# Optimization experiments

Hardware: AMD Instinct MI355X
Metric: run time of the kernel (lower is better)

## Reference

```python
import jax, jax.numpy as jnp
import numpy as np
import math

D = 1024; H = 16; HD = D // H; K = 8; NS = 512; G = D // 4
N_IN = D // 5; N_AT = int(D * 0.3); N_OUT = int(D * 0.3)
N_MO = D - N_IN - N_AT - N_OUT
M_IN = 4; M_AT = 128; M_OUT = 16; M_MO = 4; NLM_H = 16
B = 2; T = 512
T_IN = 2; T_MO = 2  # ticks_per_region: input/motor = max(2, K//8)


def _glu(z):
    a, b = jnp.split(z, 2, axis=-1)
    return a * jax.nn.sigmoid(b)


def _rms(x, eps=1e-6):
    return x * jax.lax.rsqrt(jnp.mean(x * x, axis=-1, keepdims=True) + eps)


def _ln(x, g, b, eps=1e-5):
    mu = jnp.mean(x, axis=-1, keepdims=True)
    var = jnp.mean((x - mu) ** 2, axis=-1, keepdims=True)
    return (x - mu) * jax.lax.rsqrt(var + eps) * g + b


def _nlm(tr, w, b):
    # tr: (BT, n, m); w: (m, o, n); b: (n, o) -> GLU-halved (BT, n, o/2)
    return _glu(jnp.einsum('bnm,mon->bno', tr, w) + b)


def _forward(x, Wq, Wk, Wv, Wg, W_in, ln_in_g, ln_in_b, W_at, ln_at_g, ln_at_b,
             W_out, ln_out_g, ln_out_b, W_mo, ln_mo_g, ln_mo_b, tick_embed,
             decay_out, decay_act, Wc, in_w1, in_b1, in_s0, in_tr0,
             at_w1, at_b1, at_w2, at_b2, at_s0, at_tr0,
             out_w1, out_b1, out_w2, out_b2, out_s0, out_tr0,
             mo_w1, mo_b1, mo_s0, mo_tr0,
             idx_out_l, idx_out_r, idx_act_l, idx_act_r):
    Bx, Tx, _ = x.shape
    BT = Bx * Tx
    kk = _rms((x @ Wk).reshape(Bx, Tx, H, HD))
    vv = (x @ Wv).reshape(Bx, Tx, H, HD)
    mask = jnp.tril(jnp.ones((Tx, Tx), dtype=bool))
    scale = 1.0 / math.sqrt(HD)

    state = jnp.broadcast_to(jnp.concatenate([in_s0, at_s0, out_s0, mo_s0]), (BT, D))
    tr_in = jnp.broadcast_to(in_tr0, (BT, N_IN, M_IN))
    tr_at = jnp.broadcast_to(at_tr0, (BT, N_AT, M_AT))
    tr_out = jnp.broadcast_to(out_tr0, (BT, N_OUT, M_OUT))
    tr_mo = jnp.broadcast_to(mo_tr0, (BT, N_MO, M_MO))

    alpha_out = state[:, idx_out_l] * state[:, idx_out_r]
    beta_out = jnp.ones_like(alpha_out)
    alpha_act = state[:, idx_act_l] * state[:, idx_act_r]
    beta_act = jnp.ones_like(alpha_act)
    d_out = jnp.exp(-jnp.clip(decay_out, 0.0, 15.0))
    d_act = jnp.exp(-jnp.clip(decay_act, 0.0, 15.0))

    s_in = state[:, :N_IN]
    s_at = state[:, N_IN:N_IN + N_AT]
    s_out = state[:, N_IN + N_AT:N_IN + N_AT + N_OUT]
    s_mo = state[:, N_IN + N_AT + N_OUT:]

    for t in range(K):  # fixed small tick count
        sync_act = alpha_act * jax.lax.rsqrt(beta_act)
        q = _rms((sync_act @ Wq).reshape(Bx, Tx, H, HD))
        sc = jnp.einsum('bqhd,bkhd->bhqk', q, kk) * scale
        sc = jnp.where(mask, sc, -1e30)
        attn = jnp.einsum('bhqk,bkhd->bqhd', jax.nn.softmax(sc, axis=-1), vv)
        attn = attn.reshape(BT, D) + tick_embed[t]
        gfeat = _glu(state @ Wg)

        if t < T_IN:
            pre = _ln(_glu(jnp.concatenate([attn, s_mo, gfeat], -1) @ W_in), ln_in_g, ln_in_b)
            tr_in = jnp.concatenate([tr_in[:, :, 1:], pre[:, :, None]], -1)
            s_in = _nlm(tr_in, in_w1, in_b1)[..., 0]

        pre = _ln(_glu(jnp.concatenate([s_in, attn], -1) @ W_at), ln_at_g, ln_at_b)
        tr_at = jnp.concatenate([tr_at[:, :, 1:], pre[:, :, None]], -1)
        s_at = _nlm(_nlm(tr_at, at_w1, at_b1), at_w2, at_b2)[..., 0]

        pre = _ln(_glu(jnp.concatenate([s_at, attn, gfeat], -1) @ W_out), ln_out_g, ln_out_b)
        tr_out = jnp.concatenate([tr_out[:, :, 1:], pre[:, :, None]], -1)
        s_out = _nlm(_nlm(tr_out, out_w1, out_b1), out_w2, out_b2)[..., 0]

        if t < T_MO:
            pre = _ln(_glu(jnp.concatenate([s_out, gfeat], -1) @ W_mo), ln_mo_g, ln_mo_b)
            tr_mo = jnp.concatenate([tr_mo[:, :, 1:], pre[:, :, None]], -1)
            s_mo = _nlm(tr_mo, mo_w1, mo_b1)[..., 0]

        state = jnp.concatenate([s_in, s_at, s_out, s_mo], -1)
        alpha_out = d_out * alpha_out + state[:, idx_out_l] * state[:, idx_out_r]
        beta_out = d_out * beta_out + 1.0
        alpha_act = d_act * alpha_act + state[:, idx_act_l] * state[:, idx_act_r]
        beta_act = d_act * beta_act + 1.0

    sync_out = alpha_out * jax.lax.rsqrt(beta_out)
    return (sync_out @ Wc).reshape(Bx, Tx, D)


def setup_inputs():
    key = jax.random.key(0)
    ki = iter(jax.random.split(key, 64))
    s = (3.0 ** 0.5) * (D ** -0.5) * 0.68

    def un(shape, sc):
        return jax.random.uniform(next(ki), shape, jnp.float32, -sc, sc)

    def sl(m, o, n):  # SuperLinear: w (m,o,n), b zeros (n,o)
        sc = 1.0 / math.sqrt(m + o)
        return un((m, o, n), sc), jnp.zeros((n, o), jnp.float32)

    inp = {}
    inp['x'] = jax.random.normal(next(ki), (B, T, D), jnp.float32)
    inp['Wq'] = un((NS, D), s); inp['Wk'] = un((D, D), s); inp['Wv'] = un((D, D), s)
    inp['Wg'] = un((D, 2 * G), s)
    inp['W_in'] = un((D + N_MO + G, 2 * N_IN), s)
    inp['ln_in_g'] = jnp.ones(N_IN); inp['ln_in_b'] = jnp.zeros(N_IN)
    inp['W_at'] = un((N_IN + D, 2 * N_AT), s)
    inp['ln_at_g'] = jnp.ones(N_AT); inp['ln_at_b'] = jnp.zeros(N_AT)
    inp['W_out'] = un((N_AT + D + G, 2 * N_OUT), s)
    inp['ln_out_g'] = jnp.ones(N_OUT); inp['ln_out_b'] = jnp.zeros(N_OUT)
    inp['W_mo'] = un((N_OUT + G, 2 * N_MO), s)
    inp['ln_mo_g'] = jnp.ones(N_MO); inp['ln_mo_b'] = jnp.zeros(N_MO)
    inp['tick_embed'] = jax.random.normal(next(ki), (K, D), jnp.float32) * 0.02
    inp['decay_out'] = jnp.zeros(NS, jnp.float32)
    inp['decay_act'] = jnp.zeros(NS, jnp.float32)
    inp['Wc'] = un((NS, D), s)
    inp['in_w1'], inp['in_b1'] = sl(M_IN, 2, N_IN)
    inp['in_s0'] = un((N_IN,), math.sqrt(1.0 / N_IN))
    inp['in_tr0'] = un((N_IN, M_IN), math.sqrt(1.0 / (N_IN + M_IN)))
    inp['at_w1'], inp['at_b1'] = sl(M_AT, 2 * NLM_H, N_AT)
    inp['at_w2'], inp['at_b2'] = sl(NLM_H, 2, N_AT)
    inp['at_s0'] = un((N_AT,), math.sqrt(1.0 / N_AT))
    inp['at_tr0'] = un((N_AT, M_AT), math.sqrt(1.0 / (N_AT + M_AT)))
    inp['out_w1'], inp['out_b1'] = sl(M_OUT, 2 * NLM_H, N_OUT)
    inp['out_w2'], inp['out_b2'] = sl(NLM_H, 2, N_OUT)
    inp['out_s0'] = un((N_OUT,), math.sqrt(1.0 / N_OUT))
    inp['out_tr0'] = un((N_OUT, M_OUT), math.sqrt(1.0 / (N_OUT + M_OUT)))
    inp['mo_w1'], inp['mo_b1'] = sl(M_MO, 2, N_MO)
    inp['mo_s0'] = un((N_MO,), math.sqrt(1.0 / N_MO))
    inp['mo_tr0'] = un((N_MO, M_MO), math.sqrt(1.0 / (N_MO + M_MO)))
    inp['idx_out_l'] = jax.random.permutation(next(ki), D)[:NS].astype(jnp.int32)
    inp['idx_out_r'] = jax.random.permutation(next(ki), D)[:NS].astype(jnp.int32)
    inp['idx_act_l'] = jax.random.permutation(next(ki), D)[:NS].astype(jnp.int32)
    inp['idx_act_r'] = jax.random.permutation(next(ki), D)[:NS].astype(jnp.int32)
    return inp


def reference(x, Wq, Wk, Wv, Wg, W_in, ln_in_g, ln_in_b, W_at, ln_at_g, ln_at_b,
              W_out, ln_out_g, ln_out_b, W_mo, ln_mo_g, ln_mo_b, tick_embed,
              decay_out, decay_act, Wc, in_w1, in_b1, in_s0, in_tr0,
              at_w1, at_b1, at_w2, at_b2, at_s0, at_tr0,
              out_w1, out_b1, out_w2, out_b2, out_s0, out_tr0,
              mo_w1, mo_b1, mo_s0, mo_tr0,
              idx_out_l, idx_out_r, idx_act_l, idx_act_r):
    return _forward(x, Wq, Wk, Wv, Wg, W_in, ln_in_g, ln_in_b, W_at, ln_at_g, ln_at_b,
                    W_out, ln_out_g, ln_out_b, W_mo, ln_mo_g, ln_mo_b, tick_embed,
                    decay_out, decay_act, Wc, in_w1, in_b1, in_s0, in_tr0,
                    at_w1, at_b1, at_w2, at_b2, at_s0, at_tr0,
                    out_w1, out_b1, out_w2, out_b2, out_s0, out_tr0,
                    mo_w1, mo_b1, mo_s0, mo_tr0,
                    idx_out_l, idx_out_r, idx_act_l, idx_act_r)
```

## Files before the change

kernel.cpp:

```cpp
#include <hip/hip_runtime.h>
#include <hip/hip_bf16.h>
#include <math.h>

typedef __hip_bfloat16 bf16;
typedef short v8s __attribute__((ext_vector_type(8)));
typedef float v4f __attribute__((ext_vector_type(4)));

__device__ __forceinline__ float B2F(bf16 x) { return __bfloat162float(x); }
__device__ __forceinline__ float sigm(float x) { return 1.0f / (1.0f + expf(-x)); }

__device__ __forceinline__ void split2(float v, short& hi, short& lo) {
    unsigned u = __float_as_uint(v);
    hi = (short)(u >> 16);
    float r = v - __uint_as_float(u & 0xFFFF0000u);
    bf16 l = __float2bfloat16(r);
    short ls; __builtin_memcpy(&ls, &l, 2);
    lo = ls;
}

__device__ __forceinline__ float loadAny(const void* src, size_t off, bool bf) {
    return bf ? B2F(((const bf16*)src)[off]) : ((const float*)src)[off];
}

static constexpr int D_    = 1024;
static constexpr int H_    = 16;
static constexpr int KT_   = 8;
static constexpr int NS_   = 512;
static constexpr int G_    = 256;
static constexpr int NIN_  = 204;
static constexpr int NAT_  = 307;
static constexpr int NOUT_ = 307;
static constexpr int NMO_  = 206;
static constexpr int B_    = 2;
static constexpr int T_    = 512;
static constexpr int BT_   = 1024;
static constexpr int NF_   = 41;
static constexpr int NW_   = 9;
static constexpr int NC_   = 31;

static constexpr int LAT_ = 1248;
static constexpr int LOU_ = 1600;
static constexpr int LIN_ = 1504;
static constexpr int LMO_ = 576;

struct CvtArgs { const void* src[NC_]; long long dstOff[NC_]; long long cum[NC_ + 1]; };

__global__ void detect_kernel(const void* probe, int* flag) {
    if (threadIdx.x == 0 && blockIdx.x == 0) {
        unsigned u = *(const unsigned*)probe;
        *flag = (u == 0x3F803F80u) ? 1 : 0;
    }
}

__global__ void cvt_all_kernel(CvtArgs a, float* __restrict__ dst,
                               const int* __restrict__ flag, long long total) {
    long long i0 = ((long long)blockIdx.x * 256 + threadIdx.x) * 4;
    if (i0 >= total) return;
    int lo = 0, hi = NC_;
    while (hi - lo > 1) { int mid = (lo + hi) >> 1; if (a.cum[mid] <= i0) lo = mid; else hi = mid; }
    bool bf = (*flag != 0);
    #pragma unroll
    for (int k = 0; k < 4; ++k) {
        long long i = i0 + k;
        if (i >= total) break;
        if (i >= a.cum[lo + 1]) ++lo;
        long long off = i - a.cum[lo];
        dst[a.dstOff[lo] + off] = loadAny(a.src[lo], off, bf);
    }
}

__global__ void final_any_kernel(const float* __restrict__ src, void* dst,
                                 const int* __restrict__ flag, int n) {
    int i = blockIdx.x * blockDim.x + threadIdx.x;
    if (i >= n) return;
    if (*flag) ((bf16*)dst)[i] = __float2bfloat16(src[i]);
    else       ((float*)dst)[i] = src[i];
}

__global__ void split_x_kernel(const void* __restrict__ src, const int* __restrict__ flag,
                               short* __restrict__ dh, short* __restrict__ dl, int n) {
    int i = blockIdx.x * blockDim.x + threadIdx.x;
    if (i >= n) return;
    float v = loadAny(src, i, *flag != 0);
    short h, l; split2(v, h, l);
    dh[i] = h; dl[i] = l;
}

__global__ void zeropad_kernel(short* zath, short* zatl, short* zouth, short* zoutl,
                               short* zinh, short* zinl, short* zmoh, short* zmol) {
    int r = blockIdx.x, j = threadIdx.x;
    if (j < 20)      { zath[(size_t)r * LAT_ + 1228 + j] = 0; zatl[(size_t)r * LAT_ + 1228 + j] = 0; }
    else if (j < 33) { zouth[(size_t)r * LOU_ + 1587 + (j - 20)] = 0; zoutl[(size_t)r * LOU_ + 1587 + (j - 20)] = 0; }
    else if (j < 51) { zinh[(size_t)r * LIN_ + 1486 + (j - 33)] = 0; zinl[(size_t)r * LIN_ + 1486 + (j - 33)] = 0; }
    else             { zmoh[(size_t)r * LMO_ + 563 + (j - 51)] = 0; zmol[(size_t)r * LMO_ + 563 + (j - 51)] = 0; }
}

struct TD { const void* src; long long dstOff; int K, N, ldk; };
struct TDs { TD d[NW_]; };

__global__ __launch_bounds__(256)
void transpose_split_kernel(const int* __restrict__ flag,
                            short* __restrict__ wth, short* __restrict__ wtl, TDs tds)
{
    TD d = tds.d[blockIdx.z];
    if (d.N == 0) return;
    int k0 = blockIdx.y * 32, n0 = blockIdx.x * 32;
    if (k0 >= d.ldk || n0 >= d.N) return;
    __shared__ float T[32][33];
    bool bf = (*flag != 0);
    int r = threadIdx.x >> 5, cc = threadIdx.x & 31;
    #pragma unroll
    for (int rr = 0; rr < 4; ++rr) {
        int k = k0 + r + rr * 8;
        int n = n0 + cc;
        float v = 0.f;
        if (k < d.K && n < d.N) v = loadAny(d.src, (size_t)k * d.N + n, bf);
        T[r + rr * 8][cc] = v;
    }
    __syncthreads();
    #pragma unroll
    for (int rr = 0; rr < 4; ++rr) {
        int n = n0 + r + rr * 8;
        int k = k0 + cc;
        if (n < d.N) {
            short hi, lo;
            split2(T[cc][r + rr * 8], hi, lo);
            wth[d.dstOff + (size_t)n * d.ldk + k] = hi;
            wtl[d.dstOff + (size_t)n * d.ldk + k] = lo;
        }
    }
}

__global__ __launch_bounds__(256)
void wg_pack_kernel(const void* __restrict__ src, const int* __restrict__ flag,
                    short* __restrict__ wth, short* __restrict__ wtl)
{
    int n0 = blockIdx.x * 32;
    int k0 = blockIdx.y * 32;
    __shared__ float T[32][33];
    bool bf = (*flag != 0);
    int r = threadIdx.x >> 5, cc = threadIdx.x & 31;
    int dng = n0 + cc;
    int nsrc = (dng & 1) ? (G_ + (dng >> 1)) : (dng >> 1);
    #pragma unroll
    for (int rr = 0; rr < 4; ++rr) {
        int k = k0 + r + rr * 8;
        T[r + rr * 8][cc] = loadAny(src, (size_t)k * 512 + nsrc, bf);
    }
    __syncthreads();
    #pragma unroll
    for (int rr = 0; rr < 4; ++rr) {
        int dn = n0 + r + rr * 8;
        int k = k0 + cc;
        short hi, lo;
        split2(T[cc][r + rr * 8], hi, lo);
        wth[(size_t)dn * 1024 + k] = hi;
        wtl[(size_t)dn * 1024 + k] = lo;
    }
}

__global__ void nlm_repack_kernel(const float* __restrict__ w1, const float* __restrict__ w2,
                                  int n, int Mdim,
                                  float* __restrict__ w1d, float* __restrict__ w2t) {
    int idx = blockIdx.x * blockDim.x + threadIdx.x;
    int tot1 = 8 * n * 32;
    if (idx < tot1) {
        int o = idx & 31;
        int rest = idx >> 5;
        int i = rest % n;
        int dt = rest / n;
        w1d[((size_t)dt * n + i) * 32 + o] = w1[((size_t)(Mdim - 8 + dt) * 32 + o) * n + i];
    } else if (idx < tot1 + n * 32) {
        int j = idx - tot1;
        int o = j & 31;
        int i = j >> 5;
        w2t[(size_t)i * 32 + o] = w2[(size_t)o * n + i];
    }
}

__global__ __launch_bounds__(256)
void gemm_mfma_kernel(const short* __restrict__ Ah, const short* __restrict__ Al, int lda_s,
                      const short* __restrict__ WTh, const short* __restrict__ WTl, int ldk,
                      float* __restrict__ C, int ldc, size_t pstride, int N,
                      int KC, int nCh, const int* __restrict__ flag)
{
    __shared__ short AhS[2048], AlS[2048], WhS[2048], WlS[2048];
    const int tid = threadIdx.x;
    const int lane = tid & 63;
    const int wave = tid >> 6;
    const int wm = (wave >> 1) * 32, wn = (wave & 1) * 32;
    const int m0 = blockIdx.y * 64, n0 = blockIdx.x * 64;
    const bool wlo = (*flag == 0);
    v4f acc[2][2] = {};

    const int srow = (tid >> 6) * 16 + (tid & 15);
    const int skoff = ((tid >> 4) & 3) * 8;
    const short* ArowH = Ah + (size_t)(m0 + srow) * lda_s + skoff;
    const short* ArowL = Al + (size_t)(m0 + srow) * lda_s + skoff;
    const int wrow = n0 + srow;
    const bool wv = wrow < N;
    const short* WrowH = WTh + (size_t)(wv ? wrow : 0) * ldk + skoff;
    const short* WrowL = WTl + (size_t)(wv ? wrow : 0) * ldk + skoff;

    const int aoff = ((wm >> 4) * 64 + lane) * 8;
    const int boff = ((wn >> 4) * 64 + lane) * 8;
    const int fr = lane & 15;

    const int c0 = blockIdx.z * KC;
    const int c1 = min(nCh, c0 + KC);

    v8s pAh, pAl, pWh, pWl = {};
    {
        const int k0 = c0 << 5;
        pAh = *(const v8s*)(ArowH + k0);
        pAl = *(const v8s*)(ArowL + k0);
        pWh = (v8s){};
        if (wv) pWh = *(const v8s*)(WrowH + k0);
        if (wlo && wv) pWl = *(const v8s*)(WrowL + k0);
    }

    for (int c = c0; c < c1; ++c) {
        __syncthreads();
        *(v8s*)&AhS[tid * 8] = pAh;
        *(v8s*)&AlS[tid * 8] = pAl;
        *(v8s*)&WhS[tid * 8] = pWh;
        if (wlo) *(v8s*)&WlS[tid * 8] = pWl;
        if (c + 1 < c1) {
            const int k0 = (c + 1) << 5;
            pAh = *(const v8s*)(ArowH + k0);
            pAl = *(const v8s*)(ArowL + k0);
            pWh = (v8s){};
            if (wv) pWh = *(const v8s*)(WrowH + k0);
            if (wlo && wv) pWl = *(const v8s*)(WrowL + k0);
        }
        __syncthreads();
        v8s a_h[2], a_l[2], b_h[2];
        a_h[0] = *(v8s*)&AhS[aoff];
        a_h[1] = *(v8s*)&AhS[aoff + 512];
        a_l[0] = *(v8s*)&AlS[aoff];
        a_l[1] = *(v8s*)&AlS[aoff + 512];
        b_h[0] = *(v8s*)&WhS[boff];
        b_h[1] = *(v8s*)&WhS[boff + 512];
        #pragma unroll
        for (int i = 0; i < 2; ++i)
            #pragma unroll
            for (int j = 0; j < 2; ++j) {
                acc[i][j] = __builtin_amdgcn_mfma_f32_16x16x32_bf16(a_h[i], b_h[j], acc[i][j], 0, 0, 0);
                acc[i][j] = __builtin_amdgcn_mfma_f32_16x16x32_bf16(a_l[i], b_h[j], acc[i][j], 0, 0, 0);
            }
        if (wlo) {
            v8s b_l[2];
            b_l[0] = *(v8s*)&WlS[boff];
            b_l[1] = *(v8s*)&WlS[boff + 512];
            #pragma unroll
            for (int i = 0; i < 2; ++i)
                #pragma unroll
                for (int j = 0; j < 2; ++j)
                    acc[i][j] = __builtin_amdgcn_mfma_f32_16x16x32_bf16(a_h[i], b_l[j], acc[i][j], 0, 0, 0);
        }
    }
    float* Cs = C + (size_t)blockIdx.z * pstride;
    #pragma unroll
    for (int j = 0; j < 2; ++j) {
        int col = n0 + wn + j * 16 + fr;
        if (col < N) {
            #pragma unroll
            for (int i = 0; i < 2; ++i)
                #pragma unroll
                for (int r = 0; r < 4; ++r) {
                    int row = m0 + wm + i * 16 + (lane >> 4) * 4 + r;
                    Cs[(size_t)row * ldc + col] = acc[i][j][r];
                }
        }
    }
}

__global__ __launch_bounds__(256)
void rms_kpack_kernel(const float* __restrict__ kvb,
                      short* __restrict__ kh, short* __restrict__ kl) {
    int r = blockIdx.x * 4 + (threadIdx.x >> 6);
    int d = threadIdx.x & 63;
    int h = r & 15, key = (r >> 4) & 511, b = r >> 13;
    float v = kvb[(size_t)(b * 512 + key) * 2048 + h * 64 + d];
    float ss = v * v;
    #pragma unroll
    for (int o = 32; o > 0; o >>= 1) ss += __shfl_xor(ss, o);
    v *= 1.0f / sqrtf(ss * (1.0f / 64.0f) + 1e-6f);
    short hh, ll; split2(v, hh, ll);
    int bh = b * 16 + h;
    int kc = key >> 6, t4 = (key & 63) >> 4, f = key & 15;
    int ks = d >> 5, q = (d >> 3) & 3, j = d & 7;
    size_t o_ = (size_t)bh * 32768 + kc * 4096 + (((t4 * 2 + ks) * 64 + q * 16 + f) * 8) + j;
    kh[o_] = hh; kl[o_] = ll;
}

__global__ void vpack_kernel(const float* __restrict__ kvb,
                             short* __restrict__ vh, short* __restrict__ vl) {
    int idx = blockIdx.x * blockDim.x + threadIdx.x;
    if (idx >= 32 * 512 * 64) return;
    int d = idx & 63;
    int key = (idx >> 6) & 511;
    int bh = idx >> 15;
    int b = bh >> 4, h = bh & 15;
    float v = kvb[(size_t)(b * 512 + key) * 2048 + 1024 + h * 64 + d];
    short hh, ll; split2(v, hh, ll);
    int kc = key >> 6;
    int kk2 = key & 63;
    int ks = kk2 >> 5, q = (kk2 >> 3) & 3, j = kk2 & 7;
    int t4 = d >> 4, f = d & 15;
    size_t o = (size_t)bh * 32768 + kc * 4096 + (((t4 * 2 + ks) * 64 + q * 16 + f) * 8) + j;
    vh[o] = hh; vl[o] = ll;
}

__global__ void init_state_kernel(const float* __restrict__ s_in0, const float* __restrict__ s_at0,
                                  const float* __restrict__ s_out0, const float* __restrict__ s_mo0,
                                  float* __restrict__ state,
                                  short* __restrict__ sth, short* __restrict__ stl,
                                  short* __restrict__ zath, short* __restrict__ zatl,
                                  short* __restrict__ zouth, short* __restrict__ zoutl,
                                  short* __restrict__ zinh, short* __restrict__ zinl,
                                  short* __restrict__ zmoh, short* __restrict__ zmol) {
    int idx = blockIdx.x * blockDim.x + threadIdx.x;
    if (idx >= BT_ * D_) return;
    int b = idx >> 10;
    int i = idx & (D_ - 1);
    float v;
    if (i < NIN_) v = s_in0[i];
    else if (i < NIN_ + NAT_) v = s_at0[i - NIN_];
    else if (i < NIN_ + NAT_ + NOUT_) v = s_out0[i - NIN_ - NAT_];
    else v = s_mo0[i - NIN_ - NAT_ - NOUT_];
    state[idx] = v;
    short h, l; split2(v, h, l);
    sth[idx] = h; stl[idx] = l;
    if (i < NIN_) { zath[(size_t)b * LAT_ + i] = h; zatl[(size_t)b * LAT_ + i] = l; }
    else if (i < NIN_ + NAT_) {
        zouth[(size_t)b * LOU_ + (i - NIN_)] = h; zoutl[(size_t)b * LOU_ + (i - NIN_)] = l;
    } else if (i < NIN_ + NAT_ + NOUT_) {
        zmoh[(size_t)b * LMO_ + (i - NIN_ - NAT_)] = h; zmol[(size_t)b * LMO_ + (i - NIN_ - NAT_)] = l;
    } else {
        zinh[(size_t)b * LIN_ + 1024 + (i - NIN_ - NAT_ - NOUT_)] = h;
        zinl[(size_t)b * LIN_ + 1024 + (i - NIN_ - NAT_ - NOUT_)] = l;
    }
}

__global__ void decay_kernel(const float* __restrict__ d_o, const float* __restrict__ d_a,
                             float* __restrict__ eo, float* __restrict__ ea) {
    int j = blockIdx.x * blockDim.x + threadIdx.x;
    if (j >= NS_) return;
    float x = d_o[j]; x = fminf(fmaxf(x, 0.f), 15.f); eo[j] = expf(-x);
    float y = d_a[j]; y = fminf(fmaxf(y, 0.f), 15.f); ea[j] = expf(-y);
}

__global__ void init_sync_kernel(const float* __restrict__ state,
                                 const int* __restrict__ ol, const int* __restrict__ orr,
                                 const int* __restrict__ al, const int* __restrict__ ar,
                                 float* __restrict__ ao, float* __restrict__ bo,
                                 float* __restrict__ aa, float* __restrict__ ba,
                                 short* __restrict__ sbh, short* __restrict__ sbl) {
    int idx = blockIdx.x * blockDim.x + threadIdx.x;
    if (idx >= BT_ * NS_) return;
    int b = idx >> 9;
    int j = idx & (NS_ - 1);
    const float* st = state + (size_t)b * D_;
    float vo = st[ol[j]] * st[orr[j]];
    float va = st[al[j]] * st[ar[j]];
    ao[idx] = vo; bo[idx] = 1.f;
    aa[idx] = va; ba[idx] = 1.f;
    short h, l; split2(va, h, l);
    sbh[idx] = h; sbl[idx] = l;
}

__global__ void syncupd_kernel(const float* __restrict__ state,
                               const float* __restrict__ eo, const float* __restrict__ ea,
                               const int* __restrict__ ol, const int* __restrict__ orr,
                               const int* __restrict__ al, const int* __restrict__ ar,
                               float* __restrict__ ao, float* __restrict__ bo,
                               float* __restrict__ aa, float* __restrict__ ba,
                               short* __restrict__ sbh, short* __restrict__ sbl) {
    int idx = blockIdx.x * blockDim.x + threadIdx.x;
    if (idx >= BT_ * NS_) return;
    int b = idx >> 9;
    int j = idx & (NS_ - 1);
    const float* st = state + (size_t)b * D_;
    float d = eo[j];
    ao[idx] = d * ao[idx] + st[ol[j]] * st[orr[j]];
    bo[idx] = d * bo[idx] + 1.f;
    d = ea[j];
    float a2 = d * aa[idx] + st[al[j]] * st[ar[j]];
    float b2 = d * ba[idx] + 1.f;
    aa[idx] = a2; ba[idx] = b2;
    float v = a2 / sqrtf(b2);
    short h, l; split2(v, h, l);
    sbh[idx] = h; sbl[idx] = l;
}

__global__ void syncact_split_kernel(const float* __restrict__ a, const float* __restrict__ be,
                                     short* __restrict__ oh, short* __restrict__ olo) {
    int idx = blockIdx.x * blockDim.x + threadIdx.x;
    if (idx >= BT_ * NS_) return;
    float v = a[idx] / sqrtf(be[idx]);
    short h, l; split2(v, h, l);
    oh[idx] = h; olo[idx] = l;
}

__global__ __launch_bounds__(256)
void attn_mfma_kernel(const float* __restrict__ qpart, int qsplits, size_t qps,
                      const short* __restrict__ kh_g, const short* __restrict__ kl_g,
                      const short* __restrict__ vh_g, const short* __restrict__ vl_g,
                      const float* __restrict__ te,
                      short* __restrict__ zath, short* __restrict__ zatl,
                      short* __restrict__ zouth, short* __restrict__ zoutl,
                      short* __restrict__ zinh, short* __restrict__ zinl, int wr_in)
{
    __shared__ short kksh[4096], kksl[4096];
    __shared__ short vtsh[4096], vtsl[4096];
    __shared__ short psh[4][1024], psl[4][1024];

    const int bid = blockIdx.x;
    const int bh = bid >> 3, qbk = bid & 7;
    const int b = bh >> 4, h = bh & 15;
    const int q0 = qbk * 64;
    const int tid = threadIdx.x, w = tid >> 6, lane = tid & 63;
    const int quad = lane >> 4, fr = lane & 15;

    const int qrow = q0 + w * 16 + fr;
    const size_t qoffg = ((size_t)(b * T_ + qrow)) * D_ + h * 64 + quad * 8;
    float qv[16];
    #pragma unroll
    for (int j = 0; j < 8; ++j) { qv[j] = qpart[qoffg + j]; qv[8 + j] = qpart[qoffg + 32 + j]; }
    for (int s = 1; s < qsplits; ++s) {
        const float* qp = qpart + (size_t)s * qps + qoffg;
        #pragma unroll
        for (int j = 0; j < 8; ++j) { qv[j] += qp[j]; qv[8 + j] += qp[32 + j]; }
    }
    float ss = 0.f;
    #pragma unroll
    for (int j = 0; j < 16; ++j) ss += qv[j] * qv[j];
    ss += __shfl_xor(ss, 16);
    ss += __shfl_xor(ss, 32);
    const float qsc = (1.0f / sqrtf(ss * (1.0f / 64.0f) + 1e-6f)) * 0.125f;
    v8s qh[2], ql[2];
    #pragma unroll
    for (int ks = 0; ks < 2; ++ks)
        #pragma unroll
        for (int j = 0; j < 8; ++j) {
            short hh, ll; split2(qv[ks * 8 + j] * qsc, hh, ll);
            qh[ks][j] = hh; ql[ks][j] = ll;
        }

    v4f oacc[4] = {};
    float m_[4], l_[4];
    #pragma unroll
    for (int r = 0; r < 4; ++r) { m_[r] = -INFINITY; l_[r] = 0.f; }

    const size_t kvbase = (size_t)bh * 32768;
    const int s0 = tid * 8, s1 = (tid + 256) * 8;

    v8s pk0, pk1, pkl0, pkl1, pv0, pv1, pvl0, pvl1;
    {
        const size_t cb = kvbase;
        pk0  = *(const v8s*)&kh_g[cb + s0]; pk1  = *(const v8s*)&kh_g[cb + s1];
        pkl0 = *(const v8s*)&kl_g[cb + s0]; pkl1 = *(const v8s*)&kl_g[cb + s1];
        pv0  = *(const v8s*)&vh_g[cb + s0]; pv1  = *(const v8s*)&vh_g[cb + s1];
        pvl0 = *(const v8s*)&vl_g[cb + s0]; pvl1 = *(const v8s*)&vl_g[cb + s1];
    }

    for (int c = 0; c <= qbk; ++c) {
        __syncthreads();
        *(v8s*)&kksh[s0] = pk0;  *(v8s*)&kksh[s1] = pk1;
        *(v8s*)&kksl[s0] = pkl0; *(v8s*)&kksl[s1] = pkl1;
        *(v8s*)&vtsh[s0] = pv0;  *(v8s*)&vtsh[s1] = pv1;
        *(v8s*)&vtsl[s0] = pvl0; *(v8s*)&vtsl[s1] = pvl1;
        if (c < qbk) {
            const size_t cb = kvbase + (size_t)(c + 1) * 4096;
            pk0  = *(const v8s*)&kh_g[cb + s0]; pk1  = *(const v8s*)&kh_g[cb + s1];
            pkl0 = *(const v8s*)&kl_g[cb + s0]; pkl1 = *(const v8s*)&kl_g[cb + s1];
            pv0  = *(const v8s*)&vh_g[cb + s0]; pv1  = *(const v8s*)&vh_g[cb + s1];
            pvl0 = *(const v8s*)&vl_g[cb + s0]; pvl1 = *(const v8s*)&vl_g[cb + s1];
        }
        __syncthreads();

        v4f sv[4] = {};
        #pragma unroll
        for (int ks = 0; ks < 2; ++ks) {
            #pragma unroll
            for (int t4 = 0; t4 < 4; ++t4) {
                int so = ((t4 * 2 + ks) * 64 + lane) * 8;
                v8s bh_ = *(v8s*)&kksh[so];
                v8s bl_ = *(v8s*)&kksl[so];
                sv[t4] = __builtin_amdgcn_mfma_f32_16x16x32_bf16(qh[ks], bh_, sv[t4], 0, 0, 0);
                sv[t4] = __builtin_amdgcn_mfma_f32_16x16x32_bf16(ql[ks], bh_, sv[t4], 0, 0, 0);
                sv[t4] = __builtin_amdgcn_mfma_f32_16x16x32_bf16(qh[ks], bl_, sv[t4], 0, 0, 0);
            }
        }

        const int kb = c * 64;
        #pragma unroll
        for (int r = 0; r < 4; ++r) {
            int qg = q0 + w * 16 + quad * 4 + r;
            float rm = -INFINITY;
            #pragma unroll
            for (int t4 = 0; t4 < 4; ++t4) {
                int key = kb + t4 * 16 + fr;
                float s = sv[t4][r];
                if (key > qg) s = -1e30f;
                sv[t4][r] = s;
                rm = fmaxf(rm, s);
            }
            rm = fmaxf(rm, __shfl_xor(rm, 1));
            rm = fmaxf(rm, __shfl_xor(rm, 2));
            rm = fmaxf(rm, __shfl_xor(rm, 4));
            rm = fmaxf(rm, __shfl_xor(rm, 8));
            float mn = fmaxf(m_[r], rm);
            float rs = 0.f;
            #pragma unroll
            for (int t4 = 0; t4 < 4; ++t4) {
                float p = __expf(sv[t4][r] - mn);
                sv[t4][r] = p;
                rs += p;
            }
            rs += __shfl_xor(rs, 1);
            rs += __shfl_xor(rs, 2);
            rs += __shfl_xor(rs, 4);
            rs += __shfl_xor(rs, 8);
            float al = __expf(m_[r] - mn);
            l_[r] = l_[r] * al + rs;
            m_[r] = mn;
            #pragma unroll
            for (int t4 = 0; t4 < 4; ++t4) oacc[t4][r] *= al;
            #pragma unroll
            for (int t4 = 0; t4 < 4; ++t4) {
                short hh, ll; split2(sv[t4][r], hh, ll);
                int po = (((t4 >> 1) * 4 + ((t4 & 1) * 2 + (fr >> 3))) * 16 + quad * 4 + r) * 8 + (fr & 7);
                psh[w][po] = hh;
                psl[w][po] = ll;
            }
        }

        #pragma unroll
        for (int ks = 0; ks < 2; ++ks) {
            int pa = (ks * 64 + lane) * 8;
            v8s ah_ = *(v8s*)&psh[w][pa];
            v8s al_ = *(v8s*)&psl[w][pa];
            #pragma unroll
            for (int t4 = 0; t4 < 4; ++t4) {
                int so = ((t4 * 2 + ks) * 64 + lane) * 8;
                v8s bh_ = *(v8s*)&vtsh[so];
                v8s bl_ = *(v8s*)&vtsl[so];
                oacc[t4] = __builtin_amdgcn_mfma_f32_16x16x32_bf16(ah_, bh_, oacc[t4], 0, 0, 0);
                oacc[t4] = __builtin_amdgcn_mfma_f32_16x16x32_bf16(al_, bh_, oacc[t4], 0, 0, 0);
                oacc[t4] = __builtin_amdgcn_mfma_f32_16x16x32_bf16(ah_, bl_, oacc[t4], 0, 0, 0);
            }
        }
    }

    #pragma unroll
    for (int t4 = 0; t4 < 4; ++t4) {
        float tev = te[h * 64 + t4 * 16 + fr];
        int col = h * 64 + t4 * 16 + fr;
        #pragma unroll
        for (int r = 0; r < 4; ++r) {
            int row = q0 + w * 16 + quad * 4 + r;
            size_t rb = (size_t)(b * T_ + row);
            float val = oacc[t4][r] / l_[r] + tev;
            short hh, ll; split2(val, hh, ll);
            zath[rb * LAT_ + NIN_ + col] = hh; zatl[rb * LAT_ + NIN_ + col] = ll;
            zouth[rb * LOU_ + NAT_ + col] = hh; zoutl[rb * LOU_ + NAT_ + col] = ll;
            if (wr_in) { zinh[rb * LIN_ + col] = hh; zinl[rb * LIN_ + col] = ll; }
        }
    }
}

__global__ void glu_sum_kernel(const float* __restrict__ p, int S, size_t pstride,
                               short* __restrict__ zouth, short* __restrict__ zoutl,
                               short* __restrict__ zinh, short* __restrict__ zinl,
                               short* __restrict__ zmoh, short* __restrict__ zmol, int wr2) {
    int idx = blockIdx.x * blockDim.x + threadIdx.x;
    if (idx >= BT_ * G_) return;
    int row = idx >> 8, j = idx & 255;
    float a = 0.f, bb = 0.f;
    for (int s = 0; s < S; ++s) {
        const float* pr = p + (size_t)s * pstride + (size_t)row * 512;
        a += pr[2 * j];
        bb += pr[2 * j + 1];
    }
    float gf = a * sigm(bb);
    short hh, ll; split2(gf, hh, ll);
    zouth[(size_t)row * LOU_ + 1331 + j] = hh; zoutl[(size_t)row * LOU_ + 1331 + j] = ll;
    if (wr2) {
        zinh[(size_t)row * LIN_ + 1230 + j] = hh; zinl[(size_t)row * LIN_ + 1230 + j] = ll;
        zmoh[(size_t)row * LMO_ + NOUT_ + j] = hh; zmol[(size_t)row * LMO_ + NOUT_ + j] = ll;
    }
}

__global__ __launch_bounds__(256)
void glu_ln_nlm_big_kernel(const float* __restrict__ z, size_t pstride, int n,
                           const float* __restrict__ g, const float* __restrict__ bb,
                           float* __restrict__ preBase, int t,
                           const float* __restrict__ st, const float* __restrict__ w1d,
                           const float* __restrict__ b1, const float* __restrict__ w2t,
                           const float* __restrict__ b2,
                           float* __restrict__ state, short* __restrict__ sth,
                           short* __restrict__ stl, int soff,
                           short* __restrict__ czh, short* __restrict__ czl,
                           int ldz, int catoff)
{
    __shared__ float preLDS[320];
    __shared__ float red[256];
    const int row = blockIdx.x;
    const float* zr = z + (size_t)row * 2 * n;
    float v[2];
    float lsum = 0.f;
    {
        int s = 0;
        for (int i = threadIdx.x; i < n; i += 256, ++s) {
            float a = zr[i] + zr[pstride + i] + zr[2 * pstride + i] + zr[3 * pstride + i];
            float gt = zr[n + i] + zr[pstride + n + i] + zr[2 * pstride + n + i] + zr[3 * pstride + n + i];
            float val = a * sigm(gt);
            v[s] = val;
            lsum += val;
        }
    }
    red[threadIdx.x] = lsum;
    __syncthreads();
    for (int sd = 128; sd > 0; sd >>= 1) {
        if (threadIdx.x < sd) red[threadIdx.x] += red[threadIdx.x + sd];
        __syncthreads();
    }
    float mu = red[0] / n;
    __syncthreads();
    float lss = 0.f;
    {
        int s = 0;
        for (int i = threadIdx.x; i < n; i += 256, ++s) { float dv = v[s] - mu; lss += dv * dv; }
    }
    red[threadIdx.x] = lss;
    __syncthreads();
    for (int sd = 128; sd > 0; sd >>= 1) {
        if (threadIdx.x < sd) red[threadIdx.x] += red[threadIdx.x + sd];
        __syncthreads();
    }
    float inv = 1.f / sqrtf(red[0] / n + 1e-5f);
    {
        int s = 0;
        for (int i = threadIdx.x; i < n; i += 256, ++s) {
            float pre = (v[s] - mu) * inv * g[i] + bb[i];
            preLDS[i] = pre;
            preBase[((size_t)t * BT_ + row) * n + i] = pre;
        }
    }
    __syncthreads();
    const int i_loc = threadIdx.x >> 3;
    const int og = threadIdx.x & 7;
    const int npass = (n + 31) >> 5;
    for (int p = 0; p < npass; ++p) {
        const int i = p * 32 + i_loc;
        if (i < n) {
            float4 h4;
            {
                float4 a = *((const float4*)(st + ((size_t)t * n + i) * 32) + og);
                float4 bq = *((const float4*)(b1 + (size_t)i * 32) + og);
                h4.x = a.x + bq.x; h4.y = a.y + bq.y; h4.z = a.z + bq.z; h4.w = a.w + bq.w;
            }
            for (int s = 0; s <= t; ++s) {
                float pv = (s < t) ? preBase[((size_t)s * BT_ + row) * n + i] : preLDS[i];
                float4 wq = *((const float4*)(w1d + ((size_t)(7 - t + s) * n + i) * 32) + og);
                h4.x += pv * wq.x; h4.y += pv * wq.y; h4.z += pv * wq.z; h4.w += pv * wq.w;
            }
            float4 hp;
            hp.x = __shfl_xor(h4.x, 4); hp.y = __shfl_xor(h4.y, 4);
            hp.z = __shfl_xor(h4.z, 4); hp.w = __shfl_xor(h4.w, 4);
            float h20 = 0.f, h21 = 0.f;
            if (og < 4) {
                float gv0 = h4.x * sigm(hp.x);
                float gv1 = h4.y * sigm(hp.y);
                float gv2 = h4.z * sigm(hp.z);
                float gv3 = h4.w * sigm(hp.w);
                const float4* w2v = (const float4*)(w2t + (size_t)i * 32) + og * 2;
                float4 w2a = w2v[0], w2b = w2v[1];
                h20 = gv0 * w2a.x + gv1 * w2a.z + gv2 * w2b.x + gv3 * w2b.z;
                h21 = gv0 * w2a.y + gv1 * w2a.w + gv2 * w2b.y + gv3 * w2b.w;
            }
            h20 += __shfl_xor(h20, 1); h21 += __shfl_xor(h21, 1);
            h20 += __shfl_xor(h20, 2); h21 += __shfl_xor(h21, 2);
            if (og == 0) {
                h20 += b2[i * 2]; h21 += b2[i * 2 + 1];
                float res = h20 * sigm(h21);
                size_t so = (size_t)row * D_ + soff + i;
                state[so] = res;
                short hh, ll; split2(res, hh, ll);
                sth[so] = hh; stl[so] = ll;
                czh[(size_t)row * ldz + catoff + i] = hh;
                czl[(size_t)row * ldz + catoff + i] = ll;
            }
        }
    }
}

__global__ __launch_bounds__(256)
void glu_ln_nlm_small_kernel(const float* __restrict__ z, size_t pstride, int n,
                             const float* __restrict__ g, const float* __restrict__ bb,
                             float* __restrict__ preBase, int t,
                             const float* __restrict__ tr0, const float* __restrict__ w1,
                             const float* __restrict__ b1,
                             float* __restrict__ state, short* __restrict__ sth,
                             short* __restrict__ stl, int soff,
                             short* __restrict__ czh, short* __restrict__ czl,
                             int ldz, int catoff)
{
    __shared__ float preLDS[320];
    __shared__ float red[256];
    const int row = blockIdx.x;
    const float* zr = z + (size_t)row * 2 * n;
    float v[2];
    float lsum = 0.f;
    {
        int s = 0;
        for (int i = threadIdx.x; i < n; i += 256, ++s) {
            float a = zr[i] + zr[pstride + i] + zr[2 * pstride + i] + zr[3 * pstride + i];
            float gt = zr[n + i] + zr[pstride + n + i] + zr[2 * pstride + n + i] + zr[3 * pstride + n + i];
            float val = a * sigm(gt);
            v[s] = val;
            lsum += val;
        }
    }
    red[threadIdx.x] = lsum;
    __syncthreads();
    for (int sd = 128; sd > 0; sd >>= 1) {
        if (threadIdx.x < sd) red[threadIdx.x] += red[threadIdx.x + sd];
        __syncthreads();
    }
    float mu = red[0] / n;
    __syncthreads();
    float lss = 0.f;
    {
        int s = 0;
        for (int i = threadIdx.x; i < n; i += 256, ++s) { float dv = v[s] - mu; lss += dv * dv; }
    }
    red[threadIdx.x] = lss;
    __syncthreads();
    for (int sd = 128; sd > 0; sd >>= 1) {
        if (threadIdx.x < sd) red[threadIdx.x] += red[threadIdx.x + sd];
        __syncthreads();
    }
    float inv = 1.f / sqrtf(red[0] / n + 1e-5f);
    {
        int s = 0;
        for (int i = threadIdx.x; i < n; i += 256, ++s) {
            float pre = (v[s] - mu) * inv * g[i] + bb[i];
            preLDS[i] = pre;
            preBase[((size_t)t * BT_ + row) * n + i] = pre;
        }
    }
    __syncthreads();
    for (int i = threadIdx.x; i < n; i += 256) {
        float win[4];
        if (t == 0) {
            win[0] = tr0[i * 4 + 1]; win[1] = tr0[i * 4 + 2]; win[2] = tr0[i * 4 + 3];
            win[3] = preLDS[i];
        } else {
            win[0] = tr0[i * 4 + 2]; win[1] = tr0[i * 4 + 3];
            win[2] = preBase[(size_t)row * n + i];
            win[3] = preLDS[i];
        }
        float h0 = b1[i * 2], h1 = b1[i * 2 + 1];
        #pragma unroll
        for (int mm = 0; mm < 4; ++mm) {
            h0 += win[mm] * w1[(size_t)(mm * 2 + 0) * n + i];
            h1 += win[mm] * w1[(size_t)(mm * 2 + 1) * n + i];
        }
        float res = h0 * sigm(h1);
        size_t so = (size_t)row * D_ + soff + i;
        state[so] = res;
        short hh, ll; split2(res, hh, ll);
        sth[so] = hh; stl[so] = ll;
        czh[(size_t)row * ldz + catoff + i] = hh;
        czl[(size_t)row * ldz + catoff + i] = ll;
    }
}

__global__ __launch_bounds__(256)
void static_nlm_kernel(const float* __restrict__ tr0, const float* __restrict__ w1,
                       float* __restrict__ st, int n, int Mdim)
{
    __shared__ float ws[127 * 32];
    __shared__ float trs[128];
    const int i = blockIdx.x;
    const int tid = threadIdx.x;
    const int nw = (Mdim - 1) * 32;
    for (int idx = tid; idx < nw; idx += 256)
        ws[idx] = w1[(size_t)idx * n + i];
    if (tid < Mdim) trs[tid] = tr0[(size_t)i * Mdim + tid];
    __syncthreads();
    const int t = tid >> 5, o = tid & 31;
    float h = 0.f;
    for (int j = 0; j + t + 1 < Mdim; ++j)
        h += trs[j + t + 1] * ws[j * 32 + o];
    st[((size_t)t * n + i) * 32 + o] = h;
}

extern "C" void kernel_launch(void* const* d_in, const int* in_sizes, int n_in,
                              void* d_out, int out_size, void* d_ws, size_t ws_size,
                              hipStream_t stream)
{
    const int* idx_ol = (const int*)d_in[41];
    const int* idx_or = (const int*)d_in[42];
    const int* idx_al = (const int*)d_in[43];
    const int* idx_ar = (const int*)d_in[44];

    size_t off = 0;
    auto alloc = [&](size_t ne) {
        float* r = (float*)d_ws + off;
        off += (ne + 63) & ~(size_t)63;
        return r;
    };
    int* flag = (int*)alloc(64);

    long long fcum[NF_ + 1];
    fcum[0] = 0;
    for (int i = 0; i < NF_; ++i) fcum[i + 1] = fcum[i] + in_sizes[i];
    float* stage = alloc((size_t)fcum[NF_]);
    auto SP = [&](int i) { return (const float*)(stage + fcum[i]); };

    const int cIdx[NC_] = {6, 7, 9, 10, 12, 13, 15, 16, 17, 18, 19,
                           21, 22, 23, 24, 25, 26, 27, 28, 29, 30,
                           31, 32, 33, 34, 35, 36, 37, 38, 39, 40};
    CvtArgs ca;
    long long ccum = 0;
    for (int i = 0; i < NC_; ++i) {
        int gi = cIdx[i];
        ca.src[i] = d_in[gi];
        ca.dstOff[i] = fcum[gi];
        ca.cum[i] = ccum;
        ccum += in_sizes[gi];
    }
    ca.cum[NC_] = ccum;

    const int wIdx[NW_] = {1, 2, 3, 4, 5, 8, 11, 14, 20};
    const int wK[NW_]   = {512, 1024, 1024, 1024, 1486, 1228, 1587, 563, 512};
    const int wN[NW_]   = {1024, 1024, 1024, 512, 408, 614, 614, 412, 1024};
    const int wS[NW_]   = {2, 1, 1, 4, 4, 4, 4, 4, 1};
    int ldkA[NW_];
    long long wOff[NW_];
    long long totS = 0;
    for (int i = 0; i < NW_; ++i) {
        ldkA[i] = (wK[i] + 31) & ~31;
        wOff[i] = totS;
        totS += (long long)wN[i] * ldkA[i];
    }
    short* wtH = (short*)alloc((size_t)(totS + 1) / 2 + 64);
    short* wtL = (short*)alloc((size_t)(totS + 1) / 2 + 64);

    short* xh     = (short*)alloc((size_t)BT_ * D_ / 2 + 64);
    short* xl     = (short*)alloc((size_t)BT_ * D_ / 2 + 64);
    short* sbh    = (short*)alloc((size_t)BT_ * NS_ / 2 + 64);
    short* sbl    = (short*)alloc((size_t)BT_ * NS_ / 2 + 64);
    short* sobh   = (short*)alloc((size_t)BT_ * NS_ / 2 + 64);
    short* sobl   = (short*)alloc((size_t)BT_ * NS_ / 2 + 64);
    short* sth    = (short*)alloc((size_t)BT_ * D_ / 2 + 64);
    short* stl    = (short*)alloc((size_t)BT_ * D_ / 2 + 64);
    short* khp    = (short*)alloc((size_t)32 * 512 * 64 / 2 + 64);
    short* klp    = (short*)alloc((size_t)32 * 512 * 64 / 2 + 64);
    short* vhp    = (short*)alloc((size_t)32 * 512 * 64 / 2 + 64);
    short* vlp    = (short*)alloc((size_t)32 * 512 * 64 / 2 + 64);
    short* zath   = (short*)alloc((size_t)BT_ * LAT_ / 2 + 64);
    short* zatl   = (short*)alloc((size_t)BT_ * LAT_ / 2 + 64);
    short* zouth  = (short*)alloc((size_t)BT_ * LOU_ / 2 + 64);
    short* zoutl  = (short*)alloc((size_t)BT_ * LOU_ / 2 + 64);
    short* zinh   = (short*)alloc((size_t)BT_ * LIN_ / 2 + 64);
    short* zinl   = (short*)alloc((size_t)BT_ * LIN_ / 2 + 64);
    short* zmoh   = (short*)alloc((size_t)BT_ * LMO_ / 2 + 64);
    short* zmol   = (short*)alloc((size_t)BT_ * LMO_ / 2 + 64);

    float* pbuf   = alloc((size_t)4 * BT_ * 1024);
    float* kvb    = alloc((size_t)BT_ * 2048);
    float* state  = alloc((size_t)BT_ * D_);
    float* ao     = alloc((size_t)BT_ * NS_);
    float* bo     = alloc((size_t)BT_ * NS_);
    float* aa     = alloc((size_t)BT_ * NS_);
    float* ba     = alloc((size_t)BT_ * NS_);
    float* eo     = alloc(NS_);
    float* ea     = alloc(NS_);
    float* pre_at = alloc((size_t)KT_ * BT_ * NAT_);
    float* pre_out= alloc((size_t)KT_ * BT_ * NOUT_);
    float* pre_in = alloc((size_t)2 * BT_ * NIN_);
    float* pre_mo = alloc((size_t)2 * BT_ * NMO_);
    float* st_at  = alloc((size_t)KT_ * NAT_ * 32);
    float* st_out = alloc((size_t)KT_ * NOUT_ * 32);
    float* w1d_at = alloc((size_t)8 * NAT_ * 32);
    float* w1d_out= alloc((size_t)8 * NOUT_ * 32);
    float* w2t_at = alloc((size_t)NAT_ * 32);
    float* w2t_out= alloc((size_t)NOUT_ * 32);
    float* outf   = alloc((size_t)BT_ * D_);
    (void)ws_size; (void)n_in; (void)out_size;

    detect_kernel<<<1, 64, 0, stream>>>(d_in[6], flag);
    cvt_all_kernel<<<(int)((ccum / 4 + 255) / 256) + 1, 256, 0, stream>>>(ca, stage, flag, ccum);
    zeropad_kernel<<<BT_, 64, 0, stream>>>(zath, zatl, zouth, zoutl, zinh, zinl, zmoh, zmol);
    {
        TDs tds;
        for (int i = 0; i < NW_; ++i) {
            int N = (i == 3) ? 0 : wN[i];
            tds.d[i] = TD{d_in[wIdx[i]], wOff[i], wK[i], N, ldkA[i]};
        }
        dim3 g(32, 50, NW_);
        transpose_split_kernel<<<g, 256, 0, stream>>>(flag, wtH, wtL, tds);
    }
    wg_pack_kernel<<<dim3(16, 32), 256, 0, stream>>>(d_in[4], flag, wtH + wOff[3], wtL + wOff[3]);

    const float* ln_in_g  = SP(6);
    const float* ln_in_b  = SP(7);
    const float* ln_at_g  = SP(9);
    const float* ln_at_b  = SP(10);
    const float* ln_out_g = SP(12);
    const float* ln_out_b = SP(13);
    const float* ln_mo_g  = SP(15);
    const float* ln_mo_b  = SP(16);
    const float* te       = SP(17);
    const float* dec_o    = SP(18);
    const float* dec_a    = SP(19);
    const float* in_w1    = SP(21);
    const float* in_b1    = SP(22);
    const float* in_s0    = SP(23);
    const float* in_tr0   = SP(24);
    const float* at_w1    = SP(25);
    const float* at_b1    = SP(26);
    const float* at_w2    = SP(27);
    const float* at_b2    = SP(28);
    const float* at_s0    = SP(29);
    const float* at_tr0   = SP(30);
    const float* out_w1   = SP(31);
    const float* out_b1   = SP(32);
    const float* out_w2   = SP(33);
    const float* out_b2   = SP(34);
    const float* out_s0   = SP(35);
    const float* out_tr0  = SP(36);
    const float* mo_w1    = SP(37);
    const float* mo_b1    = SP(38);
    const float* mo_s0    = SP(39);
    const float* mo_tr0   = SP(40);

    auto gemm = [&](const short* Ah, const short* Al, int lda_s, int wi,
                    float* C, int ldc) {
        int nCh = ldkA[wi] >> 5;
        int S = wS[wi];
        int KC = (nCh + S - 1) / S;
        dim3 g((wN[wi] + 63) / 64, BT_ / 64, S);
        gemm_mfma_kernel<<<g, 256, 0, stream>>>(Ah, Al, lda_s, wtH + wOff[wi], wtL + wOff[wi],
                                                ldkA[wi], C, ldc, (size_t)BT_ * ldc,
                                                wN[wi], KC, nCh, flag);
    };

    split_x_kernel<<<(BT_ * D_) / 256, 256, 0, stream>>>(d_in[0], flag, xh, xl, BT_ * D_);
    {
        dim3 g(2048 / 64, BT_ / 64, 1);
        gemm_mfma_kernel<<<g, 256, 0, stream>>>(xh, xl, 1024, wtH + wOff[1], wtL + wOff[1],
                                                1024, kvb, 2048, 0, 2048, 32, 32, flag);
    }
    rms_kpack_kernel<<<(B_ * T_ * H_) / 4, 256, 0, stream>>>(kvb, khp, klp);
    vpack_kernel<<<(32 * 512 * 64) / 256, 256, 0, stream>>>(kvb, vhp, vlp);
    init_state_kernel<<<(BT_ * D_) / 256, 256, 0, stream>>>(in_s0, at_s0, out_s0, mo_s0,
                                                            state, sth, stl,
                                                            zath, zatl, zouth, zoutl,
                                                            zinh, zinl, zmoh, zmol);
    decay_kernel<<<2, 256, 0, stream>>>(dec_o, dec_a, eo, ea);
    init_sync_kernel<<<(BT_ * NS_) / 256, 256, 0, stream>>>(state, idx_ol, idx_or, idx_al, idx_ar,
                                                            ao, bo, aa, ba, sbh, sbl);
    static_nlm_kernel<<<NAT_, 256, 0, stream>>>(at_tr0, at_w1, st_at, NAT_, 128);
    static_nlm_kernel<<<NOUT_, 256, 0, stream>>>(out_tr0, out_w1, st_out, NOUT_, 16);
    nlm_repack_kernel<<<(9 * NAT_ * 32 + 255) / 256, 256, 0, stream>>>(at_w1, at_w2, NAT_, 128,
                                                                       w1d_at, w2t_at);
    nlm_repack_kernel<<<(9 * NOUT_ * 32 + 255) / 256, 256, 0, stream>>>(out_w1, out_w2, NOUT_, 16,
                                                                        w1d_out, w2t_out);

    for (int t = 0; t < KT_; ++t) {
        gemm(sbh, sbl, 512, 0, pbuf, 1024);
        attn_mfma_kernel<<<256, 256, 0, stream>>>(pbuf, 2, (size_t)BT_ * 1024,
                                                  khp, klp, vhp, vlp, te + (size_t)t * D_,
                                                  zath, zatl, zouth, zoutl, zinh, zinl, (t < 2));
        gemm(sth, stl, 1024, 3, pbuf, 512);
        glu_sum_kernel<<<(BT_ * G_) / 256, 256, 0, stream>>>(pbuf, 4, (size_t)BT_ * 512,
                                                             zouth, zoutl, zinh, zinl,
                                                             zmoh, zmol, (t < 2));
        if (t < 2) {
            gemm(zinh, zinl, LIN_, 4, pbuf, 2 * NIN_);
            glu_ln_nlm_small_kernel<<<BT_, 256, 0, stream>>>(
                pbuf, (size_t)BT_ * 2 * NIN_, NIN_, ln_in_g, ln_in_b, pre_in, t,
                in_tr0, in_w1, in_b1, state, sth, stl, 0, zath, zatl, LAT_, 0);
        }
        gemm(zath, zatl, LAT_, 5, pbuf, 2 * NAT_);
        glu_ln_nlm_big_kernel<<<BT_, 256, 0, stream>>>(
            pbuf, (size_t)BT_ * 2 * NAT_, NAT_, ln_at_g, ln_at_b, pre_at, t,
            st_at, w1d_at, at_b1, w2t_at, at_b2, state, sth, stl, NIN_,
            zouth, zoutl, LOU_, 0);
        gemm(zouth, zoutl, LOU_, 6, pbuf, 2 * NOUT_);
        glu_ln_nlm_big_kernel<<<BT_, 256, 0, stream>>>(
            pbuf, (size_t)BT_ * 2 * NOUT_, NOUT_, ln_out_g, ln_out_b, pre_out, t,
            st_out, w1d_out, out_b1, w2t_out, out_b2, state, sth, stl, NIN_ + NAT_,
            zmoh, zmol, LMO_, 0);
        if (t < 2) {
            gemm(zmoh, zmol, LMO_, 7, pbuf, 2 * NMO_);
            glu_ln_nlm_small_kernel<<<BT_, 256, 0, stream>>>(
                pbuf, (size_t)BT_ * 2 * NMO_, NMO_, ln_mo_g, ln_mo_b, pre_mo, t,
                mo_tr0, mo_w1, mo_b1, state, sth, stl, NIN_ + NAT_ + NOUT_,
                zinh, zinl, LIN_, 1024);
        }
        syncupd_kernel<<<(BT_ * NS_) / 256, 256, 0, stream>>>(state, eo, ea, idx_ol, idx_or,
                                                              idx_al, idx_ar, ao, bo, aa, ba, sbh, sbl);
    }

    syncact_split_kernel<<<(BT_ * NS_) / 256, 256, 0, stream>>>(ao, bo, sobh, sobl);
    gemm(sobh, sobl, 512, 8, outf, 1024);
    final_any_kernel<<<(BT_ * D_) / 256, 256, 0, stream>>>(outf, d_out, flag, BT_ * D_);
}
```

Measured before the change: 1.646 ms.

## Process two rows per block in GLU-LN-NLM big kernel to reuse weights

Each block now handles two token rows. Two wavefronts do the GLU+LayerNorm with wave-level shuffle reductions instead of LDS tree reductions. In the NLM phase the per-neuron weight loads (w1d history taps, st, b1, w2) are hoisted and shared across both rows, which halves weight traffic and cuts block-level barriers. The cost is half as many blocks, so there is less parallelism to hide latency, and more registers are used for the cached float4 weights.

```diff
diff --git a/kernel.cpp b/kernel.cpp
--- a/kernel.cpp
+++ b/kernel.cpp
@@ -605,93 +605,92 @@
                            short* __restrict__ czh, short* __restrict__ czl,
                            int ldz, int catoff)
 {
-    __shared__ float preLDS[320];
-    __shared__ float red[256];
-    const int row = blockIdx.x;
-    const float* zr = z + (size_t)row * 2 * n;
-    float v[2];
-    float lsum = 0.f;
-    {
-        int s = 0;
-        for (int i = threadIdx.x; i < n; i += 256, ++s) {
+    __shared__ float preLDS[2][320];
+    const int tid = threadIdx.x;
+    const int wvid = tid >> 6, lane = tid & 63;
+    const int row0 = blockIdx.x * 2;
+
+    if (wvid < 2) {
+        const int row = row0 + wvid;
+        const float* zr = z + (size_t)row * 2 * n;
+        float v[6];
+        float lsum = 0.f;
+        int cnt = 0;
+        for (int i = lane; i < n; i += 64, ++cnt) {
             float a = zr[i] + zr[pstride + i] + zr[2 * pstride + i] + zr[3 * pstride + i];
             float gt = zr[n + i] + zr[pstride + n + i] + zr[2 * pstride + n + i] + zr[3 * pstride + n + i];
             float val = a * sigm(gt);
-            v[s] = val;
+            v[cnt] = val;
             lsum += val;
         }
-    }
-    red[threadIdx.x] = lsum;
+        #pragma unroll
+        for (int o = 32; o > 0; o >>= 1) lsum += __shfl_xor(lsum, o);
+        float mu = lsum / n;
+        float lss = 0.f;
+        for (int c = 0; c < cnt; ++c) { float dv = v[c] - mu; lss += dv * dv; }
+        #pragma unroll
+        for (int o = 32; o > 0; o >>= 1) lss += __shfl_xor(lss, o);
+        float inv = 1.f / sqrtf(lss / n + 1e-5f);
+        int c = 0;
+        for (int i = lane; i < n; i += 64, ++c) {
+            float pre = (v[c] - mu) * inv * g[i] + bb[i];
+            preLDS[wvid][i] = pre;
+            preBase[((size_t)t * BT_ + row) * n + i] = pre;
+        }
+    }
     __syncthreads();
-    for (int sd = 128; sd > 0; sd >>= 1) {
-        if (threadIdx.x < sd) red[threadIdx.x] += red[threadIdx.x + sd];
-        __syncthreads();
-    }
-    float mu = red[0] / n;
-    __syncthreads();
-    float lss = 0.f;
-    {
-        int s = 0;
-        for (int i = threadIdx.x; i < n; i += 256, ++s) { float dv = v[s] - mu; lss += dv * dv; }
-    }
-    red[threadIdx.x] = lss;
-    __syncthreads();
-    for (int sd = 128; sd > 0; sd >>= 1) {
-        if (threadIdx.x < sd) red[threadIdx.x] += red[threadIdx.x + sd];
-        __syncthreads();
-    }
-    float inv = 1.f / sqrtf(red[0] / n + 1e-5f);
-    {
-        int s = 0;
-        for (int i = threadIdx.x; i < n; i += 256, ++s) {
-            float pre = (v[s] - mu) * inv * g[i] + bb[i];
-            preLDS[i] = pre;
-            preBase[((size_t)t * BT_ + row) * n + i] = pre;
-        }
-    }
-    __syncthreads();
-    const int i_loc = threadIdx.x >> 3;
-    const int og = threadIdx.x & 7;
+
+    const int i_loc = tid >> 3;
+    const int og = tid & 7;
     const int npass = (n + 31) >> 5;
     for (int p = 0; p < npass; ++p) {
         const int i = p * 32 + i_loc;
         if (i < n) {
-            float4 h4;
-            {
-                float4 a = *((const float4*)(st + ((size_t)t * n + i) * 32) + og);
-                float4 bq = *((const float4*)(b1 + (size_t)i * 32) + og);
-                h4.x = a.x + bq.x; h4.y = a.y + bq.y; h4.z = a.z + bq.z; h4.w = a.w + bq.w;
+            float4 stq = *((const float4*)(st + ((size_t)t * n + i) * 32) + og);
+            float4 b1q = *((const float4*)(b1 + (size_t)i * 32) + og);
+            float4 wq[8];
+            for (int s = 0; s <= t; ++s)
+                wq[s] = *((const float4*)(w1d + ((size_t)(7 - t + s) * n + i) * 32) + og);
+            float4 w2a = {}, w2b = {};
+            if (og < 4) {
+                const float4* w2v = (const float4*)(w2t + (size_t)i * 32) + og * 2;
+                w2a = w2v[0]; w2b = w2v[1];
             }
-            for (int s = 0; s <= t; ++s) {
-                float pv = (s < t) ? preBase[((size_t)s * BT_ + row) * n + i] : preLDS[i];
-                float4 wq = *((const float4*)(w1d + ((size_t)(7 - t + s) * n + i) * 32) + og);
-                h4.x += pv * wq.x; h4.y += pv * wq.y; h4.z += pv * wq.z; h4.w += pv * wq.w;
-            }
-            float4 hp;
-            hp.x = __shfl_xor(h4.x, 4); hp.y = __shfl_xor(h4.y, 4);
-            hp.z = __shfl_xor(h4.z, 4); hp.w = __shfl_xor(h4.w, 4);
-            float h20 = 0.f, h21 = 0.f;
-            if (og < 4) {
-                float gv0 = h4.x * sigm(hp.x);
-                float gv1 = h4.y * sigm(hp.y);
-                float gv2 = h4.z * sigm(hp.z);
-                float gv3 = h4.w * sigm(hp.w);
-                const float4* w2v = (const float4*)(w2t + (size_t)i * 32) + og * 2;
-                float4 w2a = w2v[0], w2b = w2v[1];
-                h20 = gv0 * w2a.x + gv1 * w2a.z + gv2 * w2b.x + gv3 * w2b.z;
-                h21 = gv0 * w2a.y + gv1 * w2a.w + gv2 * w2b.y + gv3 * w2b.w;
-            }
-            h20 += __shfl_xor(h20, 1); h21 += __shfl_xor(h21, 1);
-            h20 += __shfl_xor(h20, 2); h21 += __shfl_xor(h21, 2);
-            if (og == 0) {
-                h20 += b2[i * 2]; h21 += b2[i * 2 + 1];
-                float res = h20 * sigm(h21);
-                size_t so = (size_t)row * D_ + soff + i;
-                state[so] = res;
-                short hh, ll; split2(res, hh, ll);
-                sth[so] = hh; stl[so] = ll;
-                czh[(size_t)row * ldz + catoff + i] = hh;
-                czl[(size_t)row * ldz + catoff + i] = ll;
+            #pragma unroll
+            for (int r = 0; r < 2; ++r) {
+                const int row = row0 + r;
+                float4 h4;
+                h4.x = stq.x + b1q.x; h4.y = stq.y + b1q.y;
+                h4.z = stq.z + b1q.z; h4.w = stq.w + b1q.w;
+                for (int s = 0; s <= t; ++s) {
+                    float pv = (s < t) ? preBase[((size_t)s * BT_ + row) * n + i] : preLDS[r][i];
+                    h4.x += pv * wq[s].x; h4.y += pv * wq[s].y;
+                    h4.z += pv * wq[s].z; h4.w += pv * wq[s].w;
+                }
+                float4 hp;
+                hp.x = __shfl_xor(h4.x, 4); hp.y = __shfl_xor(h4.y, 4);
+                hp.z = __shfl_xor(h4.z, 4); hp.w = __shfl_xor(h4.w, 4);
+                float h20 = 0.f, h21 = 0.f;
+                if (og < 4) {
+                    float gv0 = h4.x * sigm(hp.x);
+                    float gv1 = h4.y * sigm(hp.y);
+                    float gv2 = h4.z * sigm(hp.z);
+                    float gv3 = h4.w * sigm(hp.w);
+                    h20 = gv0 * w2a.x + gv1 * w2a.z + gv2 * w2b.x + gv3 * w2b.z;
+                    h21 = gv0 * w2a.y + gv1 * w2a.w + gv2 * w2b.y + gv3 * w2b.w;
+                }
+                h20 += __shfl_xor(h20, 1); h21 += __shfl_xor(h21, 1);
+                h20 += __shfl_xor(h20, 2); h21 += __shfl_xor(h21, 2);
+                if (og == 0) {
+                    h20 += b2[i * 2]; h21 += b2[i * 2 + 1];
+                    float res = h20 * sigm(h21);
+                    size_t so = (size_t)row * D_ + soff + i;
+                    state[so] = res;
+                    short hh, ll; split2(res, hh, ll);
+                    sth[so] = hh; stl[so] = ll;
+                    czh[(size_t)row * ldz + catoff + i] = hh;
+                    czl[(size_t)row * ldz + catoff + i] = ll;
+                }
             }
         }
     }
@@ -989,12 +988,12 @@
                 in_tr0, in_w1, in_b1, state, sth, stl, 0, zath, zatl, LAT_, 0);
         }
         gemm(zath, zatl, LAT_, 5, pbuf, 2 * NAT_);
-        glu_ln_nlm_big_kernel<<<BT_, 256, 0, stream>>>(
+        glu_ln_nlm_big_kernel<<<BT_ / 2, 256, 0, stream>>>(
             pbuf, (size_t)BT_ * 2 * NAT_, NAT_, ln_at_g, ln_at_b, pre_at, t,
             st_at, w1d_at, at_b1, w2t_at, at_b2, state, sth, stl, NIN_,
             zouth, zoutl, LOU_, 0);
         gemm(zouth, zoutl, LOU_, 6, pbuf, 2 * NOUT_);
-        glu_ln_nlm_big_kernel<<<BT_, 256, 0, stream>>>(
+        glu_ln_nlm_big_kernel<<<BT_ / 2, 256, 0, stream>>>(
             pbuf, (size_t)BT_ * 2 * NOUT_, NOUT_, ln_out_g, ln_out_b, pre_out, t,
             st_out, w1d_out, out_b1, w2t_out, out_b2, state, sth, stl, NIN_ + NAT_,
             zmoh, zmol, LMO_, 0);
```

Result: slower. 2.115 ms (+28.5%).
